# Kernel optimization log

Measured on AMD Instinct MI355X. Metric: run time of the kernel, lower is better.

Reference implementation:

```python
import jax, jax.numpy as jnp
import numpy as np

HEADS = 4
DIM_HEAD = 128
SCALE = DIM_HEAD ** (-0.5)


def setup_inputs() -> dict:
    key = jax.random.key(0)
    k1, k2 = jax.random.split(key)
    fmap = jax.random.normal(k1, (1, 256, 64, 64), dtype=jnp.float32)
    # 1x1 conv weight, no bias: [out_channels=2*heads*dim_head, in_channels=dim]
    W_qk = jax.random.normal(k2, (1024, 256), dtype=jnp.float32) * (256 ** -0.5)
    return {"fmap": fmap, "W_qk": W_qk}


def reference(fmap, W_qk):
    b, c, h, w = fmap.shape
    # 1x1 conv == channel-wise matmul
    qk = jnp.einsum('bcxy,oc->boxy', fmap, W_qk)  # [b, 2*heads*dim_head, h, w]
    q, k = jnp.split(qk, 2, axis=1)
    def to_bhxyd(t):
        # 'b (h d) x y -> b h x y d'
        return t.reshape(b, HEADS, DIM_HEAD, h, w).transpose(0, 1, 3, 4, 2)
    q = to_bhxyd(q) * SCALE
    k = to_bhxyd(k)
    sim = jnp.einsum('bhxyd,bhuvd->bhxyuv', q, k)
    sim = sim.reshape(b, HEADS, h * w, h * w)
    return jax.nn.softmax(sim, axis=-1)
```

## Files before the change

### kernel.cpp

```cpp
#include <hip/hip_runtime.h>
#include <math.h>

#define HEADS 4
#define DHEAD 128
#define NPOS  4096
#define CIN   256
#define SCALEF 0.08838834764831845f
#define LOG2E  1.4426950408889634f
#define QSCALE (SCALEF * LOG2E)

typedef _Float16 half8  __attribute__((ext_vector_type(8)));
typedef _Float16 half4  __attribute__((ext_vector_type(4)));
typedef _Float16 half2v __attribute__((ext_vector_type(2)));
typedef float    f32x4  __attribute__((ext_vector_type(4)));

#define FRAG_HEAD_HALVES (256 * 4 * 512)

__global__ __launch_bounds__(256) void cvt_kernel(const float* __restrict__ fmap,
                                                  const float* __restrict__ W,
                                                  _Float16* __restrict__ W16,
                                                  _Float16* __restrict__ fmapT) {
  if (blockIdx.x < 16) {
    int base = blockIdx.x * 16384 + threadIdx.x;
#pragma unroll
    for (int t = 0; t < 64; ++t) {
      int idx = base + t * 256;
      float v = W[idx];
      W16[idx] = (_Float16)(idx < 512 * CIN ? v * QSCALE : v);
    }
  } else {
    int tile = blockIdx.x - 16;
    int p0 = (tile >> 2) * 64, c0 = (tile & 3) * 64;
    __shared__ float t_lds[64][65];
    int tid = threadIdx.x;
#pragma unroll
    for (int t = 0; t < 16; ++t) {
      int lin = tid + t * 256;
      int r = lin >> 6, col = lin & 63;
      t_lds[r][col] = fmap[(size_t)(c0 + r) * NPOS + p0 + col];
    }
    __syncthreads();
#pragma unroll
    for (int t = 0; t < 16; ++t) {
      int lin = tid + t * 256;
      int pr = lin >> 6, cc = lin & 63;
      fmapT[(size_t)(p0 + pr) * CIN + c0 + cc] = (_Float16)t_lds[cc][pr];
    }
  }
}

__global__ __launch_bounds__(256) void proj_mfma(const _Float16* __restrict__ W16,
                                                 const _Float16* __restrict__ fmapT,
                                                 _Float16* __restrict__ qf,
                                                 _Float16* __restrict__ kf) {
  const int p0 = blockIdx.x * 64;
  const int o0 = blockIdx.y * 64 + (threadIdx.x >> 6) * 16;
  const int l = threadIdx.x & 63;
  const int lr = l & 15, lg = l >> 4;

  const f32x4 z = {0.f, 0.f, 0.f, 0.f};
  f32x4 acc[4] = {z, z, z, z};
#pragma unroll
  for (int kb = 0; kb < 8; ++kb) {
    half8 a = *(const half8*)(W16 + (size_t)(o0 + lr) * CIN + kb * 32 + lg * 8);
#pragma unroll
    for (int j = 0; j < 4; ++j) {
      half8 b = *(const half8*)(fmapT + (size_t)(p0 + j * 16 + lr) * CIN + kb * 32 + lg * 8);
      acc[j] = __builtin_amdgcn_mfma_f32_16x16x32_f16(a, b, acc[j], 0, 0, 0);
    }
  }
  const int ob = o0 + lg * 4;
  const bool isq = ob < 512;
  const int oo = isq ? ob : ob - 512;
  const int h = oo >> 7, db = oo & 127;
  const int kb2 = db >> 5;
  const int flane = ((db >> 3) & 3) * 16 + lr;
  const int e0 = db & 7;
  _Float16* dst = (isq ? qf : kf) + (size_t)h * FRAG_HEAD_HALVES;
#pragma unroll
  for (int j = 0; j < 4; ++j) {
    int pt = (p0 >> 4) + j;
    half4 v = {(_Float16)acc[j][0], (_Float16)acc[j][1],
               (_Float16)acc[j][2], (_Float16)acc[j][3]};
    *(half4*)(dst + ((size_t)pt * 4 + kb2) * 512 + flane * 8 + e0) = v;
  }
}

#define QROWS 16
#define NTIL  32

__global__ __launch_bounds__(512) void attn_mfma(const _Float16* __restrict__ qf,
                                                 const _Float16* __restrict__ kf,
                                                 float* __restrict__ out) {
  const int b = blockIdx.x;
  const int h = (b & 7) >> 1;
  const int qtile = ((b >> 3) << 1) | (b & 1);
  const int i0 = qtile * QROWS;

  const int wv = threadIdx.x >> 6;
  const int l = threadIdx.x & 63;
  const int lr = l & 15, lg = l >> 4;

  __shared__ __align__(16) _Float16 kstage[2][8][2048];
  __shared__ float red[8][16];

  const _Float16* Qf = qf + (size_t)h * FRAG_HEAD_HALVES;
  const _Float16* Kf = kf + (size_t)h * FRAG_HEAD_HALVES;

  half8 qfr[4];
#pragma unroll
  for (int kb = 0; kb < 4; ++kb)
    qfr[kb] = *(const half8*)(Qf + ((size_t)(i0 >> 4) * 4 + kb) * 512 + l * 8);

  const int jt0 = wv * NTIL;
  const _Float16* kbase = Kf + (size_t)jt0 * 2048 + l * 8;

  half2v Pst[2 * NTIL];
  float rs = 0.f;
  const f32x4 z = {0.f, 0.f, 0.f, 0.f};

#define DMA(buf, tt)                                                          \
  { const _Float16* kp_ = kbase + (size_t)(tt) * 2048;                        \
    __builtin_amdgcn_global_load_lds(                                         \
        (const __attribute__((address_space(1))) unsigned int*)(kp_),         \
        (__attribute__((address_space(3))) unsigned int*)(&kstage[buf][wv][0]), 16, 0, 0);  \
    __builtin_amdgcn_global_load_lds(                                         \
        (const __attribute__((address_space(1))) unsigned int*)(kp_ + 512),   \
        (__attribute__((address_space(3))) unsigned int*)(&kstage[buf][wv][512]), 16, 0, 0); \
    __builtin_amdgcn_global_load_lds(                                         \
        (const __attribute__((address_space(1))) unsigned int*)(kp_ + 1024),  \
        (__attribute__((address_space(3))) unsigned int*)(&kstage[buf][wv][1024]), 16, 0, 0); \
    __builtin_amdgcn_global_load_lds(                                         \
        (const __attribute__((address_space(1))) unsigned int*)(kp_ + 1536),  \
        (__attribute__((address_space(3))) unsigned int*)(&kstage[buf][wv][1536]), 16, 0, 0); }

#define COMPUTE(buf, tt)                                                      \
  { const _Float16* sp = &kstage[buf][wv][l * 8];                             \
    half8 b0 = *(const half8*)(sp);                                           \
    half8 b1 = *(const half8*)(sp + 512);                                     \
    half8 b2 = *(const half8*)(sp + 1024);                                    \
    half8 b3 = *(const half8*)(sp + 1536);                                    \
    f32x4 acc = z;                                                            \
    __builtin_amdgcn_s_setprio(1);                                            \
    acc = __builtin_amdgcn_mfma_f32_16x16x32_f16(b0, qfr[0], acc, 0, 0, 0);   \
    acc = __builtin_amdgcn_mfma_f32_16x16x32_f16(b1, qfr[1], acc, 0, 0, 0);   \
    acc = __builtin_amdgcn_mfma_f32_16x16x32_f16(b2, qfr[2], acc, 0, 0, 0);   \
    acc = __builtin_amdgcn_mfma_f32_16x16x32_f16(b3, qfr[3], acc, 0, 0, 0);   \
    __builtin_amdgcn_s_setprio(0);                                            \
    float e0 = __builtin_amdgcn_exp2f(acc[0]);                                \
    float e1 = __builtin_amdgcn_exp2f(acc[1]);                                \
    float e2 = __builtin_amdgcn_exp2f(acc[2]);                                \
    float e3 = __builtin_amdgcn_exp2f(acc[3]);                                \
    rs += (e0 + e1) + (e2 + e3);                                              \
    Pst[2 * (tt)]     = half2v{(_Float16)e0, (_Float16)e1};                   \
    Pst[2 * (tt) + 1] = half2v{(_Float16)e2, (_Float16)e3}; }

  DMA(0, 0)
#pragma unroll
  for (int tp = 0; tp < NTIL; tp += 2) {
    DMA(1, tp + 1)
    asm volatile("s_waitcnt vmcnt(4)" ::: "memory");
    COMPUTE(0, tp)
    if (tp + 2 < NTIL) {
      DMA(0, tp + 2)
      asm volatile("s_waitcnt vmcnt(4)" ::: "memory");
    } else {
      asm volatile("s_waitcnt vmcnt(0)" ::: "memory");
    }
    COMPUTE(1, tp + 1)
  }
#undef DMA
#undef COMPUTE

  rs += __shfl_xor(rs, 16);
  rs += __shfl_xor(rs, 32);
  if (l < 16) red[wv][l] = rs;
  __syncthreads();
  float s = 0.f;
#pragma unroll
  for (int w = 0; w < 8; ++w) s += red[w][lr];
  const float inv = 1.0f / s;

  float* ob = out + ((size_t)(h * NPOS + i0 + lr)) * NPOS + jt0 * 16 + lg * 4;
#pragma unroll
  for (int t = 0; t < NTIL; ++t) {
    f32x4 v;
    v[0] = (float)Pst[2 * t][0] * inv;
    v[1] = (float)Pst[2 * t][1] * inv;
    v[2] = (float)Pst[2 * t + 1][0] * inv;
    v[3] = (float)Pst[2 * t + 1][1] * inv;
    *(f32x4*)&ob[t * 16] = v;
  }
}

extern "C" void kernel_launch(void* const* d_in, const int* in_sizes, int n_in,
                              void* d_out, int out_size, void* d_ws, size_t ws_size,
                              hipStream_t stream) {
  const float* fmap = (const float*)d_in[0];
  const float* W    = (const float*)d_in[1];
  float* out = (float*)d_out;

  char* ws = (char*)d_ws;
  _Float16* qf    = (_Float16*)(ws);
  _Float16* kf    = (_Float16*)(ws + (4u << 20));
  _Float16* W16   = (_Float16*)(ws + (8u << 20));
  _Float16* fmapT = (_Float16*)(ws + (8u << 20) + (512u << 10));

  cvt_kernel<<<272, 256, 0, stream>>>(fmap, W, W16, fmapT);
  proj_mfma<<<dim3(NPOS / 64, 1024 / 64), 256, 0, stream>>>(W16, fmapT, qf, kf);
  attn_mfma<<<NPOS / QROWS * HEADS, 512, 0, stream>>>(qf, kf, out);
}
```

Measured before the change: 108.6 us.

## Fuse conversion into projection and recompute QK^T in attention instead of storing P

The fp32-to-fp16 conversion and transpose of fmap and W move into the projection kernel. It stages fmap into padded LDS and converts W in registers, which removes one kernel launch and the intermediate buffers. The attention kernel drops its 64-register probability array. It now runs the K-stream QK^T twice: a first pass accumulates the row sums, and a second pass recomputes the exponentials and writes the normalized output. This trades doubled K loads and MFMA work for lower register pressure and higher occupancy, and the projection kernel now rereads W in fp32 for every block.

```diff
diff --git a/kernel.cpp b/kernel.cpp
--- a/kernel.cpp
+++ b/kernel.cpp
@@ -13,60 +13,58 @@
 typedef _Float16 half4  __attribute__((ext_vector_type(4)));
 typedef _Float16 half2v __attribute__((ext_vector_type(2)));
 typedef float    f32x4  __attribute__((ext_vector_type(4)));
+typedef int      i32x4  __attribute__((ext_vector_type(4)));
 
 #define FRAG_HEAD_HALVES (256 * 4 * 512)
 
-__global__ __launch_bounds__(256) void cvt_kernel(const float* __restrict__ fmap,
+__global__ __launch_bounds__(256) void proj_fused(const float* __restrict__ fmap,
                                                   const float* __restrict__ W,
-                                                  _Float16* __restrict__ W16,
-                                                  _Float16* __restrict__ fmapT) {
-  if (blockIdx.x < 16) {
-    int base = blockIdx.x * 16384 + threadIdx.x;
-#pragma unroll
-    for (int t = 0; t < 64; ++t) {
-      int idx = base + t * 256;
-      float v = W[idx];
-      W16[idx] = (_Float16)(idx < 512 * CIN ? v * QSCALE : v);
-    }
-  } else {
-    int tile = blockIdx.x - 16;
-    int p0 = (tile >> 2) * 64, c0 = (tile & 3) * 64;
-    __shared__ float t_lds[64][65];
-    int tid = threadIdx.x;
-#pragma unroll
-    for (int t = 0; t < 16; ++t) {
-      int lin = tid + t * 256;
-      int r = lin >> 6, col = lin & 63;
-      t_lds[r][col] = fmap[(size_t)(c0 + r) * NPOS + p0 + col];
-    }
-    __syncthreads();
-#pragma unroll
-    for (int t = 0; t < 16; ++t) {
-      int lin = tid + t * 256;
-      int pr = lin >> 6, cc = lin & 63;
-      fmapT[(size_t)(p0 + pr) * CIN + c0 + cc] = (_Float16)t_lds[cc][pr];
-    }
-  }
-}
-
-__global__ __launch_bounds__(256) void proj_mfma(const _Float16* __restrict__ W16,
-                                                 const _Float16* __restrict__ fmapT,
-                                                 _Float16* __restrict__ qf,
-                                                 _Float16* __restrict__ kf) {
+                                                  _Float16* __restrict__ qf,
+                                                  _Float16* __restrict__ kf) {
   const int p0 = blockIdx.x * 64;
   const int o0 = blockIdx.y * 64 + (threadIdx.x >> 6) * 16;
+  const int wv = threadIdx.x >> 6;
   const int l = threadIdx.x & 63;
   const int lr = l & 15, lg = l >> 4;
 
+  __shared__ _Float16 fstage[64 * 258];
+
+  {
+    const int cb0 = wv * 64;
+#pragma unroll
+    for (int cb = 0; cb < 32; ++cb) {
+      int c = cb0 + cb * 2;
+      float f0 = fmap[(size_t)(c + 0) * NPOS + p0 + l];
+      float f1 = fmap[(size_t)(c + 1) * NPOS + p0 + l];
+      half2v hv = {(_Float16)f0, (_Float16)f1};
+      *(half2v*)&fstage[l * 258 + c] = hv;
+    }
+  }
+  __syncthreads();
+
+  const float sc = (o0 + lr) < 512 ? QSCALE : 1.0f;
   const f32x4 z = {0.f, 0.f, 0.f, 0.f};
   f32x4 acc[4] = {z, z, z, z};
 #pragma unroll
   for (int kb = 0; kb < 8; ++kb) {
-    half8 a = *(const half8*)(W16 + (size_t)(o0 + lr) * CIN + kb * 32 + lg * 8);
+    const float* wp = W + (size_t)(o0 + lr) * CIN + kb * 32 + lg * 8;
+    f32x4 w0 = *(const f32x4*)wp;
+    f32x4 w1 = *(const f32x4*)(wp + 4);
+    half8 a = {(_Float16)(w0[0] * sc), (_Float16)(w0[1] * sc),
+               (_Float16)(w0[2] * sc), (_Float16)(w0[3] * sc),
+               (_Float16)(w1[0] * sc), (_Float16)(w1[1] * sc),
+               (_Float16)(w1[2] * sc), (_Float16)(w1[3] * sc)};
 #pragma unroll
     for (int j = 0; j < 4; ++j) {
-      half8 b = *(const half8*)(fmapT + (size_t)(p0 + j * 16 + lr) * CIN + kb * 32 + lg * 8);
-      acc[j] = __builtin_amdgcn_mfma_f32_16x16x32_f16(a, b, acc[j], 0, 0, 0);
+      const _Float16* bp = &fstage[(j * 16 + lr) * 258 + kb * 32 + lg * 8];
+      i32x4 iv;
+      iv[0] = *(const int*)(bp);
+      iv[1] = *(const int*)(bp + 2);
+      iv[2] = *(const int*)(bp + 4);
+      iv[3] = *(const int*)(bp + 6);
+      half8 bfr;
+      __builtin_memcpy(&bfr, &iv, 16);
+      acc[j] = __builtin_amdgcn_mfma_f32_16x16x32_f16(a, bfr, acc[j], 0, 0, 0);
     }
   }
   const int ob = o0 + lg * 4;
@@ -115,7 +113,6 @@
   const int jt0 = wv * NTIL;
   const _Float16* kbase = Kf + (size_t)jt0 * 2048 + l * 8;
 
-  half2v Pst[2 * NTIL];
   float rs = 0.f;
   const f32x4 z = {0.f, 0.f, 0.f, 0.f};
 
@@ -134,8 +131,8 @@
         (const __attribute__((address_space(1))) unsigned int*)(kp_ + 1536),  \
         (__attribute__((address_space(3))) unsigned int*)(&kstage[buf][wv][1536]), 16, 0, 0); }
 
-#define COMPUTE(buf, tt)                                                      \
-  { const _Float16* sp = &kstage[buf][wv][l * 8];                             \
+#define QKT(buf)                                                              \
+    const _Float16* sp = &kstage[buf][wv][l * 8];                             \
     half8 b0 = *(const half8*)(sp);                                           \
     half8 b1 = *(const half8*)(sp + 512);                                     \
     half8 b2 = *(const half8*)(sp + 1024);                                    \
@@ -146,31 +143,27 @@
     acc = __builtin_amdgcn_mfma_f32_16x16x32_f16(b1, qfr[1], acc, 0, 0, 0);   \
     acc = __builtin_amdgcn_mfma_f32_16x16x32_f16(b2, qfr[2], acc, 0, 0, 0);   \
     acc = __builtin_amdgcn_mfma_f32_16x16x32_f16(b3, qfr[3], acc, 0, 0, 0);   \
-    __builtin_amdgcn_s_setprio(0);                                            \
-    float e0 = __builtin_amdgcn_exp2f(acc[0]);                                \
-    float e1 = __builtin_amdgcn_exp2f(acc[1]);                                \
-    float e2 = __builtin_amdgcn_exp2f(acc[2]);                                \
-    float e3 = __builtin_amdgcn_exp2f(acc[3]);                                \
-    rs += (e0 + e1) + (e2 + e3);                                              \
-    Pst[2 * (tt)]     = half2v{(_Float16)e0, (_Float16)e1};                   \
-    Pst[2 * (tt) + 1] = half2v{(_Float16)e2, (_Float16)e3}; }
+    __builtin_amdgcn_s_setprio(0);
+
+#define SUM(buf)                                                              \
+  { QKT(buf)                                                                  \
+    rs += (__builtin_amdgcn_exp2f(acc[0]) + __builtin_amdgcn_exp2f(acc[1]))   \
+        + (__builtin_amdgcn_exp2f(acc[2]) + __builtin_amdgcn_exp2f(acc[3])); }
 
   DMA(0, 0)
 #pragma unroll
   for (int tp = 0; tp < NTIL; tp += 2) {
     DMA(1, tp + 1)
     asm volatile("s_waitcnt vmcnt(4)" ::: "memory");
-    COMPUTE(0, tp)
+    SUM(0)
     if (tp + 2 < NTIL) {
       DMA(0, tp + 2)
       asm volatile("s_waitcnt vmcnt(4)" ::: "memory");
     } else {
       asm volatile("s_waitcnt vmcnt(0)" ::: "memory");
     }
-    COMPUTE(1, tp + 1)
-  }
-#undef DMA
-#undef COMPUTE
+    SUM(1)
+  }
 
   rs += __shfl_xor(rs, 16);
   rs += __shfl_xor(rs, 32);
@@ -182,15 +175,34 @@
   const float inv = 1.0f / s;
 
   float* ob = out + ((size_t)(h * NPOS + i0 + lr)) * NPOS + jt0 * 16 + lg * 4;
-#pragma unroll
-  for (int t = 0; t < NTIL; ++t) {
-    f32x4 v;
-    v[0] = (float)Pst[2 * t][0] * inv;
-    v[1] = (float)Pst[2 * t][1] * inv;
-    v[2] = (float)Pst[2 * t + 1][0] * inv;
-    v[3] = (float)Pst[2 * t + 1][1] * inv;
-    *(f32x4*)&ob[t * 16] = v;
-  }
+
+#define ST(buf, tt)                                                           \
+  { QKT(buf)                                                                  \
+    f32x4 v;                                                                  \
+    v[0] = __builtin_amdgcn_exp2f(acc[0]) * inv;                              \
+    v[1] = __builtin_amdgcn_exp2f(acc[1]) * inv;                              \
+    v[2] = __builtin_amdgcn_exp2f(acc[2]) * inv;                              \
+    v[3] = __builtin_amdgcn_exp2f(acc[3]) * inv;                              \
+    *(f32x4*)&ob[(tt) * 16] = v; }
+
+  DMA(0, 0)
+#pragma unroll
+  for (int tp = 0; tp < NTIL; tp += 2) {
+    DMA(1, tp + 1)
+    asm volatile("s_waitcnt vmcnt(4)" ::: "memory");
+    ST(0, tp)
+    if (tp + 2 < NTIL) {
+      DMA(0, tp + 2)
+      asm volatile("s_waitcnt vmcnt(4)" ::: "memory");
+    } else {
+      asm volatile("s_waitcnt vmcnt(0)" ::: "memory");
+    }
+    ST(1, tp + 1)
+  }
+#undef DMA
+#undef QKT
+#undef SUM
+#undef ST
 }
 
 extern "C" void kernel_launch(void* const* d_in, const int* in_sizes, int n_in,
@@ -201,12 +213,9 @@
   float* out = (float*)d_out;
 
   char* ws = (char*)d_ws;
-  _Float16* qf    = (_Float16*)(ws);
-  _Float16* kf    = (_Float16*)(ws + (4u << 20));
-  _Float16* W16   = (_Float16*)(ws + (8u << 20));
-  _Float16* fmapT = (_Float16*)(ws + (8u << 20) + (512u << 10));
-
-  cvt_kernel<<<272, 256, 0, stream>>>(fmap, W, W16, fmapT);
-  proj_mfma<<<dim3(NPOS / 64, 1024 / 64), 256, 0, stream>>>(W16, fmapT, qf, kf);
+  _Float16* qf = (_Float16*)(ws);
+  _Float16* kf = (_Float16*)(ws + (4u << 20));
+
+  proj_fused<<<dim3(NPOS / 64, 1024 / 64), 256, 0, stream>>>(fmap, W, qf, kf);
   attn_mfma<<<NPOS / QROWS * HEADS, 512, 0, stream>>>(qf, kf, out);
 }
```

New measurement: 158.1 us. +45.5%, slower.

## Process two query row tiles per block to reuse staged K fragments

Applied to the files above, without the earlier changes.

The attention kernel now handles 32 query rows per block, as two 16-row MFMA tiles, with 16 waves of 1024 threads. Each wave covers 16 key tiles instead of 32. Every K fragment loaded into LDS now feeds two MFMA chains, which halves the K global traffic per output and gives more independent MFMA work. LDS use doubles to 128KB and the register-held probability arrays grow, which may limit occupancy.

```diff
diff --git a/kernel.cpp b/kernel.cpp
--- a/kernel.cpp
+++ b/kernel.cpp
@@ -86,37 +86,41 @@
   }
 }
 
-#define QROWS 16
-#define NTIL  32
-
-__global__ __launch_bounds__(512) void attn_mfma(const _Float16* __restrict__ qf,
-                                                 const _Float16* __restrict__ kf,
-                                                 float* __restrict__ out) {
+#define QROWS 32
+#define NTIL  16
+
+__global__ __launch_bounds__(1024, 4) void attn_mfma(const _Float16* __restrict__ qf,
+                                                     const _Float16* __restrict__ kf,
+                                                     float* __restrict__ out) {
   const int b = blockIdx.x;
   const int h = (b & 7) >> 1;
-  const int qtile = ((b >> 3) << 1) | (b & 1);
-  const int i0 = qtile * QROWS;
+  const int qt = ((b >> 3) << 1) | (b & 1);
+  const int i0 = qt * QROWS;
 
   const int wv = threadIdx.x >> 6;
   const int l = threadIdx.x & 63;
   const int lr = l & 15, lg = l >> 4;
 
-  __shared__ __align__(16) _Float16 kstage[2][8][2048];
-  __shared__ float red[8][16];
+  __shared__ __align__(16) _Float16 kstage[2][16][2048];
+  __shared__ float red[16][32];
 
   const _Float16* Qf = qf + (size_t)h * FRAG_HEAD_HALVES;
   const _Float16* Kf = kf + (size_t)h * FRAG_HEAD_HALVES;
 
-  half8 qfr[4];
-#pragma unroll
-  for (int kb = 0; kb < 4; ++kb)
-    qfr[kb] = *(const half8*)(Qf + ((size_t)(i0 >> 4) * 4 + kb) * 512 + l * 8);
+  const int rt0 = i0 >> 4;
+  half8 qfrA[4], qfrB[4];
+#pragma unroll
+  for (int kb = 0; kb < 4; ++kb) {
+    qfrA[kb] = *(const half8*)(Qf + ((size_t)rt0 * 4 + kb) * 512 + l * 8);
+    qfrB[kb] = *(const half8*)(Qf + ((size_t)(rt0 + 1) * 4 + kb) * 512 + l * 8);
+  }
 
   const int jt0 = wv * NTIL;
   const _Float16* kbase = Kf + (size_t)jt0 * 2048 + l * 8;
 
-  half2v Pst[2 * NTIL];
-  float rs = 0.f;
+  half2v PA[2 * NTIL];
+  half2v PB[2 * NTIL];
+  float rsA = 0.f, rsB = 0.f;
   const f32x4 z = {0.f, 0.f, 0.f, 0.f};
 
 #define DMA(buf, tt)                                                          \
@@ -140,20 +144,31 @@
     half8 b1 = *(const half8*)(sp + 512);                                     \
     half8 b2 = *(const half8*)(sp + 1024);                                    \
     half8 b3 = *(const half8*)(sp + 1536);                                    \
-    f32x4 acc = z;                                                            \
+    f32x4 aA = z, aB = z;                                                     \
     __builtin_amdgcn_s_setprio(1);                                            \
-    acc = __builtin_amdgcn_mfma_f32_16x16x32_f16(b0, qfr[0], acc, 0, 0, 0);   \
-    acc = __builtin_amdgcn_mfma_f32_16x16x32_f16(b1, qfr[1], acc, 0, 0, 0);   \
-    acc = __builtin_amdgcn_mfma_f32_16x16x32_f16(b2, qfr[2], acc, 0, 0, 0);   \
-    acc = __builtin_amdgcn_mfma_f32_16x16x32_f16(b3, qfr[3], acc, 0, 0, 0);   \
+    aA = __builtin_amdgcn_mfma_f32_16x16x32_f16(b0, qfrA[0], aA, 0, 0, 0);    \
+    aB = __builtin_amdgcn_mfma_f32_16x16x32_f16(b0, qfrB[0], aB, 0, 0, 0);    \
+    aA = __builtin_amdgcn_mfma_f32_16x16x32_f16(b1, qfrA[1], aA, 0, 0, 0);    \
+    aB = __builtin_amdgcn_mfma_f32_16x16x32_f16(b1, qfrB[1], aB, 0, 0, 0);    \
+    aA = __builtin_amdgcn_mfma_f32_16x16x32_f16(b2, qfrA[2], aA, 0, 0, 0);    \
+    aB = __builtin_amdgcn_mfma_f32_16x16x32_f16(b2, qfrB[2], aB, 0, 0, 0);    \
+    aA = __builtin_amdgcn_mfma_f32_16x16x32_f16(b3, qfrA[3], aA, 0, 0, 0);    \
+    aB = __builtin_amdgcn_mfma_f32_16x16x32_f16(b3, qfrB[3], aB, 0, 0, 0);    \
     __builtin_amdgcn_s_setprio(0);                                            \
-    float e0 = __builtin_amdgcn_exp2f(acc[0]);                                \
-    float e1 = __builtin_amdgcn_exp2f(acc[1]);                                \
-    float e2 = __builtin_amdgcn_exp2f(acc[2]);                                \
-    float e3 = __builtin_amdgcn_exp2f(acc[3]);                                \
-    rs += (e0 + e1) + (e2 + e3);                                              \
-    Pst[2 * (tt)]     = half2v{(_Float16)e0, (_Float16)e1};                   \
-    Pst[2 * (tt) + 1] = half2v{(_Float16)e2, (_Float16)e3}; }
+    float eA0 = __builtin_amdgcn_exp2f(aA[0]);                                \
+    float eA1 = __builtin_amdgcn_exp2f(aA[1]);                                \
+    float eA2 = __builtin_amdgcn_exp2f(aA[2]);                                \
+    float eA3 = __builtin_amdgcn_exp2f(aA[3]);                                \
+    float eB0 = __builtin_amdgcn_exp2f(aB[0]);                                \
+    float eB1 = __builtin_amdgcn_exp2f(aB[1]);                                \
+    float eB2 = __builtin_amdgcn_exp2f(aB[2]);                                \
+    float eB3 = __builtin_amdgcn_exp2f(aB[3]);                                \
+    rsA += (eA0 + eA1) + (eA2 + eA3);                                         \
+    rsB += (eB0 + eB1) + (eB2 + eB3);                                         \
+    PA[2 * (tt)]     = half2v{(_Float16)eA0, (_Float16)eA1};                  \
+    PA[2 * (tt) + 1] = half2v{(_Float16)eA2, (_Float16)eA3};                  \
+    PB[2 * (tt)]     = half2v{(_Float16)eB0, (_Float16)eB1};                  \
+    PB[2 * (tt) + 1] = half2v{(_Float16)eB2, (_Float16)eB3}; }
 
   DMA(0, 0)
 #pragma unroll
@@ -172,24 +187,39 @@
 #undef DMA
 #undef COMPUTE
 
-  rs += __shfl_xor(rs, 16);
-  rs += __shfl_xor(rs, 32);
-  if (l < 16) red[wv][l] = rs;
+  rsA += __shfl_xor(rsA, 16);
+  rsA += __shfl_xor(rsA, 32);
+  rsB += __shfl_xor(rsB, 16);
+  rsB += __shfl_xor(rsB, 32);
+  if (l < 16) {
+    red[wv][l] = rsA;
+    red[wv][16 + l] = rsB;
+  }
   __syncthreads();
-  float s = 0.f;
-#pragma unroll
-  for (int w = 0; w < 8; ++w) s += red[w][lr];
-  const float inv = 1.0f / s;
-
-  float* ob = out + ((size_t)(h * NPOS + i0 + lr)) * NPOS + jt0 * 16 + lg * 4;
+  float sA = 0.f, sB = 0.f;
+#pragma unroll
+  for (int w = 0; w < 16; ++w) {
+    sA += red[w][lr];
+    sB += red[w][16 + lr];
+  }
+  const float invA = 1.0f / sA;
+  const float invB = 1.0f / sB;
+
+  float* obA = out + ((size_t)(h * NPOS + i0 + lr)) * NPOS + jt0 * 16 + lg * 4;
+  float* obB = obA + (size_t)16 * NPOS;
 #pragma unroll
   for (int t = 0; t < NTIL; ++t) {
-    f32x4 v;
-    v[0] = (float)Pst[2 * t][0] * inv;
-    v[1] = (float)Pst[2 * t][1] * inv;
-    v[2] = (float)Pst[2 * t + 1][0] * inv;
-    v[3] = (float)Pst[2 * t + 1][1] * inv;
-    *(f32x4*)&ob[t * 16] = v;
+    f32x4 vA, vB;
+    vA[0] = (float)PA[2 * t][0] * invA;
+    vA[1] = (float)PA[2 * t][1] * invA;
+    vA[2] = (float)PA[2 * t + 1][0] * invA;
+    vA[3] = (float)PA[2 * t + 1][1] * invA;
+    vB[0] = (float)PB[2 * t][0] * invB;
+    vB[1] = (float)PB[2 * t][1] * invB;
+    vB[2] = (float)PB[2 * t + 1][0] * invB;
+    vB[3] = (float)PB[2 * t + 1][1] * invB;
+    *(f32x4*)&obA[t * 16] = vA;
+    *(f32x4*)&obB[t * 16] = vB;
   }
 }
 
@@ -208,5 +238,5 @@
 
   cvt_kernel<<<272, 256, 0, stream>>>(fmap, W, W16, fmapT);
   proj_mfma<<<dim3(NPOS / 64, 1024 / 64), 256, 0, stream>>>(W16, fmapT, qf, kf);
-  attn_mfma<<<NPOS / QROWS * HEADS, 512, 0, stream>>>(qf, kf, out);
-}
+  attn_mfma<<<NPOS / QROWS * HEADS, 1024, 0, stream>>>(qf, kf, out);
+}
```

Measured after the change: 149.4 us. +37.6%, slower.
